# Performance work log

Measured on AMD Instinct MI355X. Metric: run time of the kernel, lower is better.

## Reference

```python
import jax, jax.numpy as jnp
import numpy as np

K = 20          # neighbors
EPS = 1e-5      # BN eps
SLOPE = 0.2     # LeakyReLU slope


def _bn_params(key, c):
    k1, k2, k3, k4 = jax.random.split(key, 4)
    gamma = jax.random.uniform(k1, (c,)) + 0.5
    beta = jax.random.normal(k2, (c,)) * 0.1
    mean = jax.random.normal(k3, (c,)) * 0.1
    var = jax.random.uniform(k4, (c,)) + 0.5
    return jnp.stack([gamma, beta, mean, var])  # [4, c]


def setup_inputs() -> dict:
    key = jax.random.key(0)
    ks = jax.random.split(key, 20)
    s = 0.05
    return {
        "x": jax.random.normal(ks[0], (16, 3, 2048), dtype=jnp.float32),
        "W1": jax.random.normal(ks[1], (64, 6)) * s,
        "bn1": _bn_params(ks[2], 64),
        "W2": jax.random.normal(ks[3], (64, 128)) * s,
        "bn2": _bn_params(ks[4], 64),
        "W3": jax.random.normal(ks[5], (128, 128)) * s,
        "bn3": _bn_params(ks[6], 128),
        "W4": jax.random.normal(ks[7], (256, 256)) * s,
        "bn4": _bn_params(ks[8], 256),
        "W5": jax.random.normal(ks[9], (1024, 512)) * s,
        "bn5": _bn_params(ks[10], 1024),
        "Wl1": jax.random.normal(ks[11], (512, 2048)) * s,
        "bn6": _bn_params(ks[12], 512),
        "Wl2": jax.random.normal(ks[13], (256, 512)) * s,
        "bl2": jax.random.normal(ks[14], (256,)) * s,
        "bn7": _bn_params(ks[15], 256),
        "Wl3": jax.random.normal(ks[16], (40, 256)) * s,
        "bl3": jax.random.normal(ks[17], (40,)) * s,
    }


def _knn_idx(xt, k):
    # xt: [B, N, C]; returns [B, N, k] indices of nearest neighbors (incl. self)
    sq = jnp.sum(xt * xt, axis=-1)                       # [B, N]
    inner = jnp.einsum("bnc,bmc->bnm", xt, xt)           # [B, N, N]
    neg_dist = 2.0 * inner - sq[:, :, None] - sq[:, None, :]
    _, idx = jax.lax.top_k(neg_dist, k)
    return idx


def _bn_act(h, bn):
    # eval-mode batchnorm over last axis + LeakyReLU
    g, b, m, v = bn[0], bn[1], bn[2], bn[3]
    h = (h - m) * (g * jax.lax.rsqrt(v + EPS)) + b
    return jnp.where(h >= 0, h, SLOPE * h)


def _edge_conv(xt, W, bn, k):
    # xt: [B, N, C] channels-last; W: [O, 2C]
    idx = _knn_idx(xt, k)                                # [B, N, k]
    nb = jax.vmap(lambda f, i: f[i])(xt, idx)            # [B, N, k, C]
    ctr = jnp.broadcast_to(xt[:, :, None, :], nb.shape)
    feat = jnp.concatenate([nb - ctr, ctr], axis=-1)     # [B, N, k, 2C]
    h = jnp.einsum("bnkc,oc->bnko", feat, W)             # 1x1 conv
    h = _bn_act(h, bn)
    return jnp.max(h, axis=2)                            # [B, N, O]


def reference(x, W1, bn1, W2, bn2, W3, bn3, W4, bn4, W5, bn5,
              Wl1, bn6, Wl2, bl2, bn7, Wl3, bl3):
    xt = jnp.transpose(x, (0, 2, 1))                     # [B, N, 3]
    x1 = _edge_conv(xt, W1, bn1, K)                      # [B, N, 64]
    x2 = _edge_conv(x1, W2, bn2, K)                      # [B, N, 64]
    x3 = _edge_conv(x2, W3, bn3, K)                      # [B, N, 128]
    x4 = _edge_conv(x3, W4, bn4, K)                      # [B, N, 256]
    cat = jnp.concatenate([x1, x2, x3, x4], axis=-1)     # [B, N, 512]
    h = jnp.einsum("bnc,oc->bno", cat, W5)               # [B, N, 1024]
    h = _bn_act(h, bn5)
    hmax = jnp.max(h, axis=1)                            # [B, 1024]
    havg = jnp.mean(h, axis=1)                           # [B, 1024]
    h = jnp.concatenate([hmax, havg], axis=-1)           # [B, 2048]
    h = _bn_act(h @ Wl1.T, bn6)                          # [B, 512] (dropout = eval no-op)
    h = _bn_act(h @ Wl2.T + bl2, bn7)                    # [B, 256]
    return h @ Wl3.T + bl3                               # [B, 40]
```

## Files before the change

### kernel.cpp

```cpp
#include <hip/hip_runtime.h>
#include <hip/hip_bf16.h>

#define BB 16
#define NN 2048
#define PP (BB*NN)
#define KNN 20

typedef __hip_bfloat16 bf16;
typedef unsigned short u16;
typedef unsigned int u32;
typedef __attribute__((ext_vector_type(8))) short s8v;
typedef __attribute__((ext_vector_type(4))) float f4v;

__device__ __forceinline__ float bu2f(u16 u){ return __uint_as_float(((u32)u) << 16); }
__device__ __forceinline__ float lo16(u32 u){ return __uint_as_float(u << 16); }
__device__ __forceinline__ float hi16(u32 u){ return __uint_as_float(u & 0xffff0000u); }
__device__ __forceinline__ u16 f2bu(float f){ bf16 h = __float2bfloat16(f); return *(u16*)&h; }
__device__ __forceinline__ float lrelu(float h){ return (h >= 0.f) ? h : 0.2f*h; }

__device__ __forceinline__ u32 f2key(float f){
  u32 u = __float_as_uint(f);
  return (u & 0x80000000u) ? ~u : (u | 0x80000000u);
}
__device__ __forceinline__ float key2f(u32 k){
  u32 u = (k & 0x80000000u) ? (k & 0x7FFFFFFFu) : ~k;
  return __uint_as_float(u);
}

template<bool BF> __device__ __forceinline__ float wget(const void* p, size_t i){
  return BF ? bu2f(((const u16*)p)[i]) : ((const float*)p)[i];
}
template<bool BF> __device__ __forceinline__ void wload8(const void* p, size_t base, float w[8]){
  if (BF){
    const uint4 u = *(const uint4*)((const u16*)p + base);
    w[0]=lo16(u.x); w[1]=hi16(u.x); w[2]=lo16(u.y); w[3]=hi16(u.y);
    w[4]=lo16(u.z); w[5]=hi16(u.z); w[6]=lo16(u.w); w[7]=hi16(u.w);
  } else {
    const float4* f = (const float4*)((const float*)p + base);
    float4 a = f[0], b = f[1];
    w[0]=a.x; w[1]=a.y; w[2]=a.z; w[3]=a.w; w[4]=b.x; w[5]=b.y; w[6]=b.z; w[7]=b.w;
  }
}

__device__ __forceinline__ f4v mfma16(s8v a, s8v b, f4v c){
  return __builtin_amdgcn_mfma_f32_16x16x32_bf16(a, b, c, 0, 0, 0);
}

template<bool BF> __device__ __forceinline__ void loadFragHL(const void* p, size_t base,
                                                             s8v& hi, s8v& lo){
  if (BF){
    hi = *(const s8v*)((const u16*)p + base);
  } else {
    float w[8]; wload8<false>(p, base, w);
    #pragma unroll
    for (int i = 0; i < 8; ++i){
      u16 hb = f2bu(w[i]);
      hi[i] = (short)hb;
      lo[i] = (short)f2bu(w[i] - bu2f(hb));
    }
  }
}
template<bool BF> __device__ __forceinline__ s8v loadFragR(const void* p, size_t base){
  if (BF){
    return *(const s8v*)((const u16*)p + base);
  } else {
    float w[8]; wload8<false>(p, base, w);
    s8v r;
    #pragma unroll
    for (int i = 0; i < 8; ++i) r[i] = (short)f2bu(w[i]);
    return r;
  }
}
template<bool BF, bool PRE> __device__ __forceinline__ s8v loadW(const void* p, size_t base){
  if (PRE) return *(const s8v*)((const u16*)p + base);
  else     return loadFragR<BF>(p, base);
}

__device__ __forceinline__ void topk_ins(float d, u32 id, float (&tv)[KNN], u32 (&ti)[KNN]){
  float pv = 0.f; u32 pi = 0u; bool cp = false;
  #pragma unroll
  for (int t = 0; t < KNN; ++t){
    bool c = (tv[t] < d);
    float ov = tv[t]; u32 oi = ti[t];
    tv[t] = c ? (cp ? pv : d) : tv[t];
    ti[t] = c ? (cp ? pi : id) : ti[t];
    pv = ov; pi = oi; cp = c;
  }
}

__global__ void k_detect(const u16* __restrict__ xr, int* __restrict__ flag){
  __shared__ int cnt;
  if (threadIdx.x == 0) cnt = 0;
  __syncthreads();
  float v = bu2f(xr[threadIdx.x * 2]);
  float a = fabsf(v);
  int ok = (a > 1e-6f && a < 1e6f) ? 1 : 0;
  atomicAdd(&cnt, ok);
  __syncthreads();
  if (threadIdx.x == 0) flag[0] = (cnt >= 160) ? 1 : 0;
}

__global__ void k_wconv(const int* __restrict__ FLAG, const void* __restrict__ src,
                        u16* __restrict__ dst, int n){
  int i = blockIdx.x*256 + threadIdx.x;
  if (i >= n) return;
  dst[i] = FLAG[0] ? ((const u16*)src)[i] : f2bu(((const float*)src)[i]);
}

template<bool BF>
__global__ void k_prep(const int* __restrict__ FLAG, const void* __restrict__ x,
                       float* __restrict__ XT, float* __restrict__ SQ,
                       u32* __restrict__ hmaxk, float* __restrict__ hsum){
  if (FLAG[0] != (BF ? 1 : 0)) return;
  int i = blockIdx.x*256 + threadIdx.x;
  if (i >= PP) return;
  int b = i / NN, n = i - b*NN;
  float s = 0.f;
  #pragma unroll
  for (int c = 0; c < 3; ++c){
    float v = wget<BF>(x, ((size_t)b*3 + c)*NN + n);
    XT[(size_t)i*3 + c] = v;
    s += v*v;
  }
  SQ[i] = s;
  if (i < BB*1024){ hmaxk[i] = 0u; hsum[i] = 0.f; }
}

template<int Cin>
__global__ void k_sq(const u16* __restrict__ xin, float* __restrict__ SQ){
  int i = blockIdx.x*256 + threadIdx.x;
  if (i >= PP) return;
  const u32* r = (const u32*)(xin + (size_t)i*Cin);
  float s = 0.f;
  for (int c = 0; c < Cin/2; ++c){
    u32 u = r[c];
    float a = lo16(u), b = hi16(u);
    s += a*a; s += b*b;
  }
  SQ[i] = s;
}

template<int C, int TC>
__global__ __launch_bounds__(256) void k_knn(const float* __restrict__ xin,
                                             const float* __restrict__ SQ,
                                             u16* __restrict__ IDX){
  __shared__ float cf[4][TC*C];
  __shared__ float csqv[4][TC];
  __shared__ float tvL[4][KNN][64];
  __shared__ u16   tiL[4][KNN][64];
  const int tid = threadIdx.x, w = tid >> 6, lane = tid & 63;
  const int b = blockIdx.y;
  const int q = blockIdx.x*64 + lane;
  const int j0 = w * 512;

  float qf[C];
  const float* xq = xin + ((size_t)b*NN + q)*C;
  #pragma unroll
  for (int c = 0; c < C; ++c) qf[c] = xq[c];
  const float sqq = SQ[b*NN + q];

  float tv[KNN]; u32 ti[KNN];
  #pragma unroll
  for (int t = 0; t < KNN; ++t){ tv[t] = -INFINITY; ti[t] = 0; }

  for (int t0 = 0; t0 < 512; t0 += TC){
    __syncthreads();
    const float* src = xin + ((size_t)b*NN + j0 + t0)*C;
    for (int k = lane; k < TC*C; k += 64) cf[w][k] = src[k];
    for (int k = lane; k < TC; k += 64) csqv[w][k] = SQ[b*NN + j0 + t0 + k];
    __syncthreads();
    for (int j = 0; j < TC; ++j){
      float dot = 0.f;
      #pragma unroll
      for (int c = 0; c < C; ++c) dot += qf[c]*cf[w][j*C + c];
      float d = 2.f*dot - sqq - csqv[w][j];
      if (d > tv[KNN-1]) topk_ins(d, (u32)(j0 + t0 + j), tv, ti);
    }
  }
  #pragma unroll
  for (int t = 0; t < KNN; ++t){ tvL[w][t][lane] = tv[t]; tiL[w][t][lane] = (u16)ti[t]; }
  __syncthreads();
  if (tid < 64){
    int p0=0,p1=0,p2=0,p3=0;
    u16* op = IDX + ((size_t)b*NN + q)*KNN;
    for (int t = 0; t < KNN; ++t){
      float v0 = tvL[0][p0][tid], v1 = tvL[1][p1][tid], v2 = tvL[2][p2][tid], v3 = tvL[3][p3][tid];
      int bs = 0; float bv = v0;
      if (v1 > bv){ bv = v1; bs = 1; }
      if (v2 > bv){ bv = v2; bs = 2; }
      if (v3 > bv){ bv = v3; bs = 3; }
      u16 bi;
      if      (bs == 0){ bi = tiL[0][p0][tid]; p0++; }
      else if (bs == 1){ bi = tiL[1][p1][tid]; p1++; }
      else if (bs == 2){ bi = tiL[2][p2][tid]; p2++; }
      else             { bi = tiL[3][p3][tid]; p3++; }
      op[t] = bi;
    }
  }
}

template<int C>
__global__ __launch_bounds__(256) void k_knn_mfma(const u16* __restrict__ xin,
                                                  const float* __restrict__ SQ,
                                                  u16* __restrict__ IDX){
  __shared__ float tvL[KNN][256];
  __shared__ u16   tiL[KNN][256];
  const int tid = threadIdx.x, w = tid >> 6, lane = tid & 63;
  const int quad = lane >> 4, n = lane & 15;
  const int seg = w & 1, qg = w >> 1;
  const int b = blockIdx.y;
  const int q = blockIdx.x*32 + qg*16 + n;
  const int cbase = seg * (NN/2);
  const u16* Xb = xin + (size_t)b*NN*C;

  s8v bfrag[C/32];
  #pragma unroll
  for (int kc = 0; kc < C/32; ++kc)
    bfrag[kc] = *(const s8v*)(Xb + (size_t)q*C + kc*32 + quad*8);
  const float sqq = SQ[b*NN + q];

  float tv[KNN]; u32 ti[KNN];
  #pragma unroll
  for (int t = 0; t < KNN; ++t){ tv[t] = -INFINITY; ti[t] = 0; }

  s8v afr[C/32], afn[C/32];
  #pragma unroll
  for (int kc = 0; kc < C/32; ++kc)
    afr[kc] = *(const s8v*)(Xb + (size_t)(cbase + n)*C + kc*32 + quad*8);

  for (int ct = cbase; ct < cbase + NN/2; ct += 16){
    int ctn = (ct + 16 < cbase + NN/2) ? (ct + 16) : cbase;
    #pragma unroll
    for (int kc = 0; kc < C/32; ++kc)
      afn[kc] = *(const s8v*)(Xb + (size_t)(ctn + n)*C + kc*32 + quad*8);
    f4v sqc = *(const f4v*)&SQ[b*NN + ct + quad*4];
    f4v acc = {0.f, 0.f, 0.f, 0.f};
    #pragma unroll
    for (int kc = 0; kc < C/32; ++kc)
      acc = mfma16(afr[kc], bfrag[kc], acc);
    #pragma unroll
    for (int r = 0; r < 4; ++r){
      float d = 2.f*acc[r] - sqq - sqc[r];
      if (d > tv[KNN-1]) topk_ins(d, (u32)(ct + quad*4 + r), tv, ti);
    }
    #pragma unroll
    for (int kc = 0; kc < C/32; ++kc) afr[kc] = afn[kc];
  }
  #pragma unroll
  for (int t = 0; t < KNN; ++t){ tvL[t][tid] = tv[t]; tiL[t][tid] = (u16)ti[t]; }
  __syncthreads();

  if (tid < 32){
    int mn = tid & 15, mqg = tid >> 4;
    int mq = blockIdx.x*32 + mqg*16 + mn;
    int p[8] = {0,0,0,0,0,0,0,0};
    u16* op = IDX + ((size_t)b*NN + mq)*KNN;
    for (int t = 0; t < KNN; ++t){
      float bv = -INFINITY; int bs = 0; u16 bi = 0xFFFF;
      #pragma unroll
      for (int s = 0; s < 8; ++s){
        int col = mqg*128 + (s >> 2)*64 + (s & 3)*16 + mn;
        float v = tvL[p[s]][col];
        u16  ii = tiL[p[s]][col];
        if (v > bv || (v == bv && ii < bi)){ bv = v; bs = s; bi = ii; }
      }
      op[t] = bi; p[bs]++;
    }
  }
}

template<bool BF>
__global__ __launch_bounds__(256) void k_ec1(const int* __restrict__ FLAG,
                    const float* __restrict__ XT,
                    const u16* __restrict__ IDX1, const void* __restrict__ W1,
                    const void* __restrict__ bn1, u16* __restrict__ x1out){
  if (FLAG[0] != (BF ? 1 : 0)) return;
  __shared__ float nbx[4][21][3];
  __shared__ float W1s[384];
  __shared__ float bn1s[256];
  __shared__ u16   idxL[4][KNN];
  const int tid = threadIdx.x;
  const int g0 = blockIdx.x*4, b = g0 / NN;
  for (int k = tid; k < 384; k += 256) W1s[k] = wget<BF>(W1, k);
  if (tid < 256) bn1s[tid] = wget<BF>(bn1, tid);
  if (tid < 80){ int pt = tid/KNN, t = tid%KNN; idxL[pt][t] = IDX1[(size_t)(g0+pt)*KNN + t]; }
  __syncthreads();
  for (int k = tid; k < 4*21*3; k += 256){
    int row = k/3, c = k - row*3;
    int pt = row/21, slot = row - pt*21;
    int m = (slot < KNN) ? (int)idxL[pt][slot] : (g0 + pt - b*NN);
    nbx[pt][slot][c] = XT[((size_t)b*NN + m)*3 + c];
  }
  __syncthreads();
  int pt = tid >> 6, o = tid & 63;
  float wa0 = W1s[o*6], wa1 = W1s[o*6+1], wa2 = W1s[o*6+2];
  float wb0 = W1s[o*6+3], wb1 = W1s[o*6+4], wb2 = W1s[o*6+5];
  float pmax = -INFINITY;
  #pragma unroll
  for (int t = 0; t < KNN; ++t)
    pmax = fmaxf(pmax, nbx[pt][t][0]*wa0 + nbx[pt][t][1]*wa1 + nbx[pt][t][2]*wa2);
  float po = nbx[pt][20][0]*wa0 + nbx[pt][20][1]*wa1 + nbx[pt][20][2]*wa2;
  float qo = nbx[pt][20][0]*wb0 + nbx[pt][20][1]*wb1 + nbx[pt][20][2]*wb2;
  float h = pmax - po + qo;
  float sc = bn1s[o] / sqrtf(bn1s[192+o] + 1e-5f);
  h = (h - bn1s[128+o])*sc + bn1s[64+o];
  x1out[(size_t)(g0+pt)*64 + o] = f2bu(lrelu(h));
}

template<int O_, bool BF>
__global__ __launch_bounds__(256, 2) void k_ec(const int* __restrict__ FLAG,
                    const u16* __restrict__ xin, const u16* __restrict__ idx,
                    const void* __restrict__ W, const void* __restrict__ bn,
                    u16* __restrict__ xout){
  if (FLAG[0] != (BF ? 1 : 0)) return;
  __shared__ __align__(16) u16 ANu[16*24*72];
  __shared__ u16 idxL[16][KNN];
  const int tid = threadIdx.x, wv = tid >> 6, lane = tid & 63;
  const int quad = lane >> 4, n = lane & 15;
  const int g0 = blockIdx.x*16, b = g0 / NN, n0 = g0 - b*NN;

  for (int k = tid; k < 16*KNN; k += 256){
    int pt = k/KNN, t = k - pt*KNN;
    idxL[pt][t] = idx[(size_t)(g0+pt)*KNN + t];
  }
  __syncthreads();
  u32* ANw = (u32*)ANu;
  for (int k = tid; k < 384*32; k += 256){
    int row = k >> 5, pr = k & 31;
    int pt = row/24, r = row - pt*24;
    int m = (r < KNN) ? (int)idxL[pt][r] : (n0 + pt);
    ANw[row*36 + pr] = ((const u32*)(xin + ((size_t)b*NN + m)*64))[pr];
  }
  __syncthreads();

  s8v aself[2];
  #pragma unroll
  for (int kc = 0; kc < 2; ++kc)
    aself[kc] = *(const s8v*)&ANu[((lane&15)*24 + 20)*72 + kc*32 + quad*8];

  for (int tt = wv; tt < O_/16; tt += 4){
    const int o = tt*16 + n;
    s8v bah[2], bal[2];
    f4v accq;
    {
      f4v tq = {0.f,0.f,0.f,0.f};
      {
        s8v bbh[2], bbl[2];
        #pragma unroll
        for (int kc = 0; kc < 2; ++kc)
          loadFragHL<BF>(W, (size_t)o*128 + 64 + kc*32 + quad*8, bbh[kc], bbl[kc]);
        #pragma unroll
        for (int kc = 0; kc < 2; ++kc){
          tq = mfma16(aself[kc], bbh[kc], tq);
          if (!BF) tq = mfma16(aself[kc], bbl[kc], tq);
        }
      }
      #pragma unroll
      for (int kc = 0; kc < 2; ++kc)
        loadFragHL<BF>(W, (size_t)o*128 + kc*32 + quad*8, bah[kc], bal[kc]);
      f4v uq = {0.f,0.f,0.f,0.f};
      #pragma unroll
      for (int kc = 0; kc < 2; ++kc){
        uq = mfma16(aself[kc], bah[kc], uq);
        if (!BF) uq = mfma16(aself[kc], bal[kc], uq);
      }
      accq = tq - uq;
    }
    float g  = wget<BF>(bn, o),        be = wget<BF>(bn, O_+o),
          mu = wget<BF>(bn, 2*O_+o),   va = wget<BF>(bn, 3*O_+o);
    float sc = g / sqrtf(va + 1e-5f);

    #pragma unroll 2
    for (int pt = 0; pt < 16; ++pt){
      s8v a0[2], a1[2];
      #pragma unroll
      for (int kc = 0; kc < 2; ++kc){
        a0[kc] = *(const s8v*)&ANu[(pt*24 + (lane&15))*72 + kc*32 + quad*8];
        a1[kc] = *(const s8v*)&ANu[(pt*24 + 16 + (lane&7))*72 + kc*32 + quad*8];
      }
      f4v c0 = {0.f,0.f,0.f,0.f}, c1 = {0.f,0.f,0.f,0.f};
      #pragma unroll
      for (int kc = 0; kc < 2; ++kc){
        c0 = mfma16(a0[kc], bah[kc], c0);
        c1 = mfma16(a1[kc], bah[kc], c1);
        if (!BF){
          c0 = mfma16(a0[kc], bal[kc], c0);
          c1 = mfma16(a1[kc], bal[kc], c1);
        }
      }
      float pm = fmaxf(fmaxf(fmaxf(c0[0],c0[1]), fmaxf(c0[2],c0[3])),
                       fmaxf(fmaxf(c1[0],c1[1]), fmaxf(c1[2],c1[3])));
      pm = fmaxf(pm, __shfl_xor(pm, 16));
      pm = fmaxf(pm, __shfl_xor(pm, 32));
      if (quad == (pt >> 2)){
        float h = pm + accq[pt & 3];
        h = (h - mu)*sc + be;
        xout[(size_t)(g0+pt)*O_ + o] = f2bu(lrelu(h));
      }
    }
  }
}

#define PTS 16
template<bool BF, bool PRE>
__global__ __launch_bounds__(512, 1)
void k_w5f(const int* __restrict__ FLAG,
      const float* __restrict__ XT,
      const u16* __restrict__ IDX1, const u16* __restrict__ x2g, const u16* __restrict__ x3g,
      const u16* __restrict__ IDX4,
      const void* __restrict__ W1, const void* __restrict__ bn1,
      const void* __restrict__ W4, const void* __restrict__ bn4,
      const void* __restrict__ W5, const void* __restrict__ bn5,
      u32* __restrict__ hmaxk, float* __restrict__ hsum){
  if (FLAG[0] != (BF ? 1 : 0)) return;
  __shared__ __align__(16) u16 ANu[PTS*24*136];
  __shared__ __align__(16) u16 xsu[PTS*520];
  __shared__ float xtn[PTS][21][3];
  __shared__ u16   idx1L[PTS][KNN], idx4L[PTS][KNN];
  __shared__ float W1s[384], bn1s[256], bn4s[1024];
  const int tid = threadIdx.x, wv = tid >> 6, lane = tid & 63;
  const int quad = lane >> 4, n = lane & 15;
  const int g0 = blockIdx.x*PTS, b = g0 / NN, n0 = g0 - b*NN;

  for (int k = tid; k < PTS*KNN; k += 512){
    int pt = k/KNN, t = k - pt*KNN;
    idx1L[pt][t] = IDX1[(size_t)(g0+pt)*KNN + t];
    idx4L[pt][t] = IDX4[(size_t)(g0+pt)*KNN + t];
  }
  if (tid < 384) W1s[tid] = wget<BF>(W1, tid);
  if (tid < 256) bn1s[tid] = wget<BF>(bn1, tid);
  for (int k = tid; k < 1024; k += 512) bn4s[k] = wget<BF>(bn4, k);
  __syncthreads();

  u32* ANw = (u32*)ANu;
  for (int k = tid; k < PTS*24*64; k += 512){
    int row = k >> 6, pr = k & 63;
    int pt = row/24, r = row - pt*24;
    int m = (r < KNN) ? (int)idx4L[pt][r] : (n0 + pt);
    ANw[(pt*24 + r)*68 + pr] = ((const u32*)(x3g + ((size_t)b*NN + m)*128))[pr];
  }
  for (int k = tid; k < PTS*21*3; k += 512){
    int row = k/3, c = k - row*3;
    int pt = row/21, slot = row - pt*21;
    int m = (slot < KNN) ? (int)idx1L[pt][slot] : (n0 + pt);
    xtn[pt][slot][c] = XT[((size_t)b*NN + m)*3 + c];
  }
  u32* xsw = (u32*)xsu;
  for (int k = tid; k < PTS*32; k += 512){
    int pt = k >> 5, c2 = k & 31;
    xsw[pt*260 + 32 + c2] = ((const u32*)(x2g + (size_t)(g0+pt)*64))[c2];
  }
  for (int k = tid; k < PTS*64; k += 512){
    int pt = k >> 6, c2 = k & 63;
    xsw[pt*260 + 64 + c2] = ((const u32*)(x3g + (size_t)(g0+pt)*128))[c2];
  }
  __syncthreads();

  #pragma unroll
  for (int hh = 0; hh < PTS*64/512; ++hh){
    int k = tid + hh*512;
    int pt = k >> 6, o = k & 63;
    float wa0 = W1s[o*6], wa1 = W1s[o*6+1], wa2 = W1s[o*6+2];
    float wb0 = W1s[o*6+3], wb1 = W1s[o*6+4], wb2 = W1s[o*6+5];
    float pmax = -INFINITY;
    #pragma unroll
    for (int t = 0; t < KNN; ++t)
      pmax = fmaxf(pmax, xtn[pt][t][0]*wa0 + xtn[pt][t][1]*wa1 + xtn[pt][t][2]*wa2);
    float po = xtn[pt][20][0]*wa0 + xtn[pt][20][1]*wa1 + xtn[pt][20][2]*wa2;
    float qo = xtn[pt][20][0]*wb0 + xtn[pt][20][1]*wb1 + xtn[pt][20][2]*wb2;
    float h = pmax - po + qo;
    float sc = bn1s[o] / sqrtf(bn1s[192+o] + 1e-5f);
    h = (h - bn1s[128+o])*sc + bn1s[64+o];
    xsu[pt*520 + o] = f2bu(lrelu(h));
  }

  {
    s8v aself[4];
    #pragma unroll
    for (int kc = 0; kc < 4; ++kc)
      aself[kc] = *(const s8v*)&ANu[((lane&15)*24 + 20)*136 + kc*32 + quad*8];

    #pragma unroll 1
    for (int i = 0; i < 2; ++i){
      const int o0 = (wv*2 + i)*16;
      const size_t wrow = (size_t)(o0 + n)*256;
      s8v bah[4];
      f4v accq;
      {
        f4v tq = {0.f,0.f,0.f,0.f};
        #pragma unroll
        for (int kc = 0; kc < 4; ++kc){
          s8v bb = loadW<BF,PRE>(W4, wrow + 128 + kc*32 + quad*8);
          tq = mfma16(aself[kc], bb, tq);
        }
        #pragma unroll
        for (int kc = 0; kc < 4; ++kc)
          bah[kc] = loadW<BF,PRE>(W4, wrow + kc*32 + quad*8);
        f4v uq = {0.f,0.f,0.f,0.f};
        #pragma unroll
        for (int kc = 0; kc < 4; ++kc)
          uq = mfma16(aself[kc], bah[kc], uq);
        accq = tq - uq;
      }
      #pragma unroll 2
      for (int pt = 0; pt < PTS; ++pt){
        s8v a0[4], a1[4];
        #pragma unroll
        for (int kc = 0; kc < 4; ++kc){
          a0[kc] = *(const s8v*)&ANu[(pt*24 + (lane&15))*136 + kc*32 + quad*8];
          a1[kc] = *(const s8v*)&ANu[(pt*24 + 16 + (lane&7))*136 + kc*32 + quad*8];
        }
        f4v c0 = {0.f,0.f,0.f,0.f}, c1 = {0.f,0.f,0.f,0.f};
        #pragma unroll
        for (int kc = 0; kc < 4; ++kc){
          c0 = mfma16(a0[kc], bah[kc], c0);
          c1 = mfma16(a1[kc], bah[kc], c1);
        }
        float pm = fmaxf(fmaxf(fmaxf(c0[0],c0[1]), fmaxf(c0[2],c0[3])),
                         fmaxf(fmaxf(c1[0],c1[1]), fmaxf(c1[2],c1[3])));
        pm = fmaxf(pm, __shfl_xor(pm, 16));
        pm = fmaxf(pm, __shfl_xor(pm, 32));
        if (quad == (pt >> 2)){
          float h = pm + accq[pt & 3];
          int o = o0 + n;
          float sc = bn4s[o] / sqrtf(bn4s[768+o] + 1e-5f);
          h = (h - bn4s[512+o])*sc + bn4s[256+o];
          xsu[pt*520 + 256 + o] = f2bu(lrelu(h));
        }
      }
    }
  }
  __syncthreads();

  {
    #pragma unroll 1
    for (int i = 0; i < 8; ++i){
      const int o = (wv*8 + i)*16 + n;
      const size_t wrow = (size_t)o * 512;
      f4v acc = {0.f,0.f,0.f,0.f};
      #pragma unroll
      for (int kc = 0; kc < 16; ++kc){
        s8v av = *(const s8v*)&xsu[(lane&15)*520 + kc*32 + quad*8];
        s8v bh = loadW<BF,PRE>(W5, wrow + kc*32 + quad*8);
        acc = mfma16(av, bh, acc);
      }
      float g = wget<BF>(bn5, o), be = wget<BF>(bn5, 1024+o),
            mu = wget<BF>(bn5, 2048+o), va = wget<BF>(bn5, 3072+o);
      float sc = g / sqrtf(va + 1e-5f);
      float lm = -INFINITY, ls = 0.f;
      #pragma unroll
      for (int r = 0; r < 4; ++r){
        float h = (acc[r] - mu)*sc + be;
        h = lrelu(h);
        lm = fmaxf(lm, h); ls += h;
      }
      lm = fmaxf(lm, __shfl_xor(lm, 16));
      ls = ls + __shfl_xor(ls, 16);
      lm = fmaxf(lm, __shfl_xor(lm, 32));
      ls = ls + __shfl_xor(ls, 32);
      if (quad == 0){
        atomicMax(&hmaxk[b*1024 + o], f2key(lm));
        atomicAdd(&hsum[b*1024 + o], ls);
      }
    }
  }
}

template<bool BF>
__global__ __launch_bounds__(512) void k_head(const int* __restrict__ FLAG,
                    const u32* __restrict__ hmaxk, const float* __restrict__ hsum,
                    const void* __restrict__ Wl1, const void* __restrict__ bn6,
                    const void* __restrict__ Wl2, const void* __restrict__ bl2,
                    const void* __restrict__ bn7,
                    const void* __restrict__ Wl3, const void* __restrict__ bl3,
                    void* __restrict__ out){
  if (FLAG[0] != (BF ? 1 : 0)) return;
  __shared__ float hc[2048];
  __shared__ float h2s[512];
  __shared__ float h3s[256];
  int b = blockIdx.x, tid = threadIdx.x;
  for (int k = tid; k < 1024; k += 512){
    hc[k]        = key2f(hmaxk[b*1024 + k]);
    hc[1024 + k] = hsum[b*1024 + k] * (1.0f/2048.0f);
  }
  __syncthreads();
  {
    float acc = 0.f;
    for (int cc = 0; cc < 2048; cc += 8){
      float w[8];
      wload8<BF>(Wl1, (size_t)tid*2048 + cc, w);
      #pragma unroll
      for (int u = 0; u < 8; ++u) acc += w[u]*hc[cc+u];
    }
    float g = wget<BF>(bn6, tid), be = wget<BF>(bn6, 512+tid),
          mu = wget<BF>(bn6, 1024+tid), va = wget<BF>(bn6, 1536+tid);
    float sc = g / sqrtf(va + 1e-5f);
    h2s[tid] = lrelu((acc - mu)*sc + be);
  }
  __syncthreads();
  if (tid < 256){
    float acc = 0.f;
    for (int cc = 0; cc < 512; cc += 8){
      float w[8];
      wload8<BF>(Wl2, (size_t)tid*512 + cc, w);
      #pragma unroll
      for (int u = 0; u < 8; ++u) acc += w[u]*h2s[cc+u];
    }
    acc += wget<BF>(bl2, tid);
    float g = wget<BF>(bn7, tid), be = wget<BF>(bn7, 256+tid),
          mu = wget<BF>(bn7, 512+tid), va = wget<BF>(bn7, 768+tid);
    float sc = g / sqrtf(va + 1e-5f);
    h3s[tid] = lrelu((acc - mu)*sc + be);
  }
  __syncthreads();
  if (tid < 40){
    float acc = 0.f;
    for (int cc = 0; cc < 256; cc += 8){
      float w[8];
      wload8<BF>(Wl3, (size_t)tid*256 + cc, w);
      #pragma unroll
      for (int u = 0; u < 8; ++u) acc += w[u]*h3s[cc+u];
    }
    acc += wget<BF>(bl3, tid);
    if (BF) ((u16*)out)[b*40 + tid] = f2bu(acc);
    else    ((float*)out)[b*40 + tid] = acc;
  }
}

extern "C" void kernel_launch(void* const* d_in, const int* in_sizes, int n_in,
                              void* d_out, int out_size, void* d_ws, size_t ws_size,
                              hipStream_t stream){
  const void* x   = d_in[0];
  const void* W1  = d_in[1];
  const void* bn1 = d_in[2];
  const void* W2  = d_in[3];
  const void* bn2 = d_in[4];
  const void* W3  = d_in[5];
  const void* bn3 = d_in[6];
  const void* W4  = d_in[7];
  const void* bn4 = d_in[8];
  const void* W5  = d_in[9];
  const void* bn5 = d_in[10];
  const void* Wl1 = d_in[11];
  const void* bn6 = d_in[12];
  const void* Wl2 = d_in[13];
  const void* bl2 = d_in[14];
  const void* bn7 = d_in[15];
  const void* Wl3 = d_in[16];
  const void* bl3 = d_in[17];

  char* base = (char*)d_ws;
  int*   FLAG  = (int*)  (base + 0);
  float* XT    = (float*)(base + 256);
  float* SQ    = (float*)(base + 393472);
  u32*   HMAXK = (u32*)  (base + 524544);
  float* HSUM  = (float*)(base + 590080);
  u16*   IDX1  = (u16*)  (base + 655616);
  u16*   IDX   = (u16*)  (base + 1966336);
  u16*   X2    = (u16*)  (base + 3277056);
  u16*   X3    = (u16*)  (base + 7471360);
  u16*   X1    = X3;
  u16*   W4B   = (u16*)  (base + 15859968);
  u16*   W5B   = (u16*)  (base + 15991040);
  const bool pre = (ws_size >= (size_t)17039616);

  dim3 knnG1(NN/64, BB);
  dim3 knnGM(NN/32, BB);

  k_detect<<<1, 256, 0, stream>>>((const u16*)x, FLAG);

  if (pre){
    k_wconv<<<(65536 + 255)/256, 256, 0, stream>>>(FLAG, W4, W4B, 65536);
    k_wconv<<<(524288 + 255)/256, 256, 0, stream>>>(FLAG, W5, W5B, 524288);
  }

  k_prep<true ><<<PP/256, 256, 0, stream>>>(FLAG, x, XT, SQ, HMAXK, HSUM);
  k_prep<false><<<PP/256, 256, 0, stream>>>(FLAG, x, XT, SQ, HMAXK, HSUM);

  k_knn<3,128><<<knnG1, 256, 0, stream>>>(XT, SQ, IDX1);
  k_ec1<true ><<<PP/4, 256, 0, stream>>>(FLAG, XT, IDX1, W1, bn1, X1);
  k_ec1<false><<<PP/4, 256, 0, stream>>>(FLAG, XT, IDX1, W1, bn1, X1);

  k_sq<64><<<PP/256, 256, 0, stream>>>(X1, SQ);
  k_knn_mfma<64><<<knnGM, 256, 0, stream>>>(X1, SQ, IDX);
  k_ec<64,true ><<<PP/16, 256, 0, stream>>>(FLAG, X1, IDX, W2, bn2, X2);
  k_ec<64,false><<<PP/16, 256, 0, stream>>>(FLAG, X1, IDX, W2, bn2, X2);

  k_sq<64><<<PP/256, 256, 0, stream>>>(X2, SQ);
  k_knn_mfma<64><<<knnGM, 256, 0, stream>>>(X2, SQ, IDX);
  k_ec<128,true ><<<PP/16, 256, 0, stream>>>(FLAG, X2, IDX, W3, bn3, X3);
  k_ec<128,false><<<PP/16, 256, 0, stream>>>(FLAG, X2, IDX, W3, bn3, X3);

  k_sq<128><<<PP/256, 256, 0, stream>>>(X3, SQ);
  k_knn_mfma<128><<<knnGM, 256, 0, stream>>>(X3, SQ, IDX);

  if (pre){
    k_w5f<true ,true ><<<PP/PTS, 512, 0, stream>>>(FLAG, XT, IDX1, X2, X3, IDX,
                                                   W1, bn1, W4B, bn4, W5B, bn5, HMAXK, HSUM);
    k_w5f<false,true ><<<PP/PTS, 512, 0, stream>>>(FLAG, XT, IDX1, X2, X3, IDX,
                                                   W1, bn1, W4B, bn4, W5B, bn5, HMAXK, HSUM);
  } else {
    k_w5f<true ,false><<<PP/PTS, 512, 0, stream>>>(FLAG, XT, IDX1, X2, X3, IDX,
                                                   W1, bn1, W4, bn4, W5, bn5, HMAXK, HSUM);
    k_w5f<false,false><<<PP/PTS, 512, 0, stream>>>(FLAG, XT, IDX1, X2, X3, IDX,
                                                   W1, bn1, W4, bn4, W5, bn5, HMAXK, HSUM);
  }

  k_head<true ><<<BB, 512, 0, stream>>>(FLAG, HMAXK, HSUM, Wl1, bn6, Wl2, bl2, bn7, Wl3, bl3, d_out);
  k_head<false><<<BB, 512, 0, stream>>>(FLAG, HMAXK, HSUM, Wl1, bn6, Wl2, bl2, bn7, Wl3, bl3, d_out);
}
```

Measured before the change: 2.012 ms.

## Pack kNN distance and index into one u32 key; pre-convert W2/W3 to bf16

The MFMA kNN kernel now keeps a single 32-bit key per candidate: an order-preserving distance key with its low 11 bits replaced by the inverted column index. This halves top-k register state and shared-memory traffic and makes the merge a plain unsigned compare. The cost is distance precision truncated to about 21 bits, which can change tie ordering for near-equal distances. Separately, W2 and W3 are converted to bf16 once into workspace so the edge-conv kernels load pre-converted fragments and skip the lo-part MFMAs on the fp32 path, when the workspace is large enough.

Measured after the change: 1.706 ms. 15.2% less time.

```diff
diff --git a/kernel.cpp b/kernel.cpp
--- a/kernel.cpp
+++ b/kernel.cpp
@@ -85,6 +85,16 @@
     tv[t] = c ? (cp ? pv : d) : tv[t];
     ti[t] = c ? (cp ? pi : id) : ti[t];
     pv = ov; pi = oi; cp = c;
+  }
+}
+__device__ __forceinline__ void topk_insp(u32 pk, u32 (&tv)[KNN]){
+  u32 pv = 0u; bool cp = false;
+  #pragma unroll
+  for (int t = 0; t < KNN; ++t){
+    bool c = (tv[t] < pk);
+    u32 ov = tv[t];
+    tv[t] = c ? (cp ? pv : pk) : tv[t];
+    pv = ov; cp = c;
   }
 }
 
@@ -203,8 +213,7 @@
 __global__ __launch_bounds__(256) void k_knn_mfma(const u16* __restrict__ xin,
                                                   const float* __restrict__ SQ,
                                                   u16* __restrict__ IDX){
-  __shared__ float tvL[KNN][256];
-  __shared__ u16   tiL[KNN][256];
+  __shared__ u32 tvL[KNN][256];
   const int tid = threadIdx.x, w = tid >> 6, lane = tid & 63;
   const int quad = lane >> 4, n = lane & 15;
   const int seg = w & 1, qg = w >> 1;
@@ -219,9 +228,9 @@
     bfrag[kc] = *(const s8v*)(Xb + (size_t)q*C + kc*32 + quad*8);
   const float sqq = SQ[b*NN + q];
 
-  float tv[KNN]; u32 ti[KNN];
-  #pragma unroll
-  for (int t = 0; t < KNN; ++t){ tv[t] = -INFINITY; ti[t] = 0; }
+  u32 tv[KNN];
+  #pragma unroll
+  for (int t = 0; t < KNN; ++t) tv[t] = 0u;
 
   s8v afr[C/32], afn[C/32];
   #pragma unroll
@@ -241,13 +250,14 @@
     #pragma unroll
     for (int r = 0; r < 4; ++r){
       float d = 2.f*acc[r] - sqq - sqc[r];
-      if (d > tv[KNN-1]) topk_ins(d, (u32)(ct + quad*4 + r), tv, ti);
+      u32 pk = (f2key(d) & 0xFFFFF800u) | (2047u - (u32)(ct + quad*4 + r));
+      if (pk > tv[KNN-1]) topk_insp(pk, tv);
     }
     #pragma unroll
     for (int kc = 0; kc < C/32; ++kc) afr[kc] = afn[kc];
   }
   #pragma unroll
-  for (int t = 0; t < KNN; ++t){ tvL[t][tid] = tv[t]; tiL[t][tid] = (u16)ti[t]; }
+  for (int t = 0; t < KNN; ++t) tvL[t][tid] = tv[t];
   __syncthreads();
 
   if (tid < 32){
@@ -256,15 +266,14 @@
     int p[8] = {0,0,0,0,0,0,0,0};
     u16* op = IDX + ((size_t)b*NN + mq)*KNN;
     for (int t = 0; t < KNN; ++t){
-      float bv = -INFINITY; int bs = 0; u16 bi = 0xFFFF;
+      u32 bv = 0u; int bs = 0;
       #pragma unroll
       for (int s = 0; s < 8; ++s){
         int col = mqg*128 + (s >> 2)*64 + (s & 3)*16 + mn;
-        float v = tvL[p[s]][col];
-        u16  ii = tiL[p[s]][col];
-        if (v > bv || (v == bv && ii < bi)){ bv = v; bs = s; bi = ii; }
-      }
-      op[t] = bi; p[bs]++;
+        u32 v = tvL[p[s]][col];
+        if (v > bv){ bv = v; bs = s; }
+      }
+      op[t] = (u16)(2047u - (bv & 2047u)); p[bs]++;
     }
   }
 }
@@ -307,7 +316,7 @@
   x1out[(size_t)(g0+pt)*64 + o] = f2bu(lrelu(h));
 }
 
-template<int O_, bool BF>
+template<int O_, bool BF, bool PRE>
 __global__ __launch_bounds__(256, 2) void k_ec(const int* __restrict__ FLAG,
                     const u16* __restrict__ xin, const u16* __restrict__ idx,
                     const void* __restrict__ W, const void* __restrict__ bn,
@@ -342,7 +351,22 @@
     const int o = tt*16 + n;
     s8v bah[2], bal[2];
     f4v accq;
-    {
+    if (PRE){
+      f4v tq = {0.f,0.f,0.f,0.f};
+      #pragma unroll
+      for (int kc = 0; kc < 2; ++kc){
+        s8v bb = *(const s8v*)((const u16*)W + (size_t)o*128 + 64 + kc*32 + quad*8);
+        tq = mfma16(aself[kc], bb, tq);
+      }
+      #pragma unroll
+      for (int kc = 0; kc < 2; ++kc)
+        bah[kc] = *(const s8v*)((const u16*)W + (size_t)o*128 + kc*32 + quad*8);
+      f4v uq = {0.f,0.f,0.f,0.f};
+      #pragma unroll
+      for (int kc = 0; kc < 2; ++kc)
+        uq = mfma16(aself[kc], bah[kc], uq);
+      accq = tq - uq;
+    } else {
       f4v tq = {0.f,0.f,0.f,0.f};
       {
         s8v bbh[2], bbl[2];
@@ -383,7 +407,7 @@
       for (int kc = 0; kc < 2; ++kc){
         c0 = mfma16(a0[kc], bah[kc], c0);
         c1 = mfma16(a1[kc], bah[kc], c1);
-        if (!BF){
+        if (!BF && !PRE){
           c0 = mfma16(a0[kc], bal[kc], c0);
           c1 = mfma16(a1[kc], bal[kc], c1);
         }
@@ -662,7 +686,10 @@
   u16*   X1    = X3;
   u16*   W4B   = (u16*)  (base + 15859968);
   u16*   W5B   = (u16*)  (base + 15991040);
-  const bool pre = (ws_size >= (size_t)17039616);
+  u16*   W2B   = (u16*)  (base + 17039616);
+  u16*   W3B   = (u16*)  (base + 17056000);
+  const bool pre  = (ws_size >= (size_t)17039616);
+  const bool pre2 = (ws_size >= (size_t)17088768);
 
   dim3 knnG1(NN/64, BB);
   dim3 knnGM(NN/32, BB);
@@ -673,6 +700,10 @@
     k_wconv<<<(65536 + 255)/256, 256, 0, stream>>>(FLAG, W4, W4B, 65536);
     k_wconv<<<(524288 + 255)/256, 256, 0, stream>>>(FLAG, W5, W5B, 524288);
   }
+  if (pre2){
+    k_wconv<<<(8192 + 255)/256, 256, 0, stream>>>(FLAG, W2, W2B, 8192);
+    k_wconv<<<(16384 + 255)/256, 256, 0, stream>>>(FLAG, W3, W3B, 16384);
+  }
 
   k_prep<true ><<<PP/256, 256, 0, stream>>>(FLAG, x, XT, SQ, HMAXK, HSUM);
   k_prep<false><<<PP/256, 256, 0, stream>>>(FLAG, x, XT, SQ, HMAXK, HSUM);
@@ -683,13 +714,23 @@
 
   k_sq<64><<<PP/256, 256, 0, stream>>>(X1, SQ);
   k_knn_mfma<64><<<knnGM, 256, 0, stream>>>(X1, SQ, IDX);
-  k_ec<64,true ><<<PP/16, 256, 0, stream>>>(FLAG, X1, IDX, W2, bn2, X2);
-  k_ec<64,false><<<PP/16, 256, 0, stream>>>(FLAG, X1, IDX, W2, bn2, X2);
+  if (pre2){
+    k_ec<64,true ,true ><<<PP/16, 256, 0, stream>>>(FLAG, X1, IDX, W2B, bn2, X2);
+    k_ec<64,false,true ><<<PP/16, 256, 0, stream>>>(FLAG, X1, IDX, W2B, bn2, X2);
+  } else {
+    k_ec<64,true ,false><<<PP/16, 256, 0, stream>>>(FLAG, X1, IDX, W2, bn2, X2);
+    k_ec<64,false,false><<<PP/16, 256, 0, stream>>>(FLAG, X1, IDX, W2, bn2, X2);
+  }
 
   k_sq<64><<<PP/256, 256, 0, stream>>>(X2, SQ);
   k_knn_mfma<64><<<knnGM, 256, 0, stream>>>(X2, SQ, IDX);
-  k_ec<128,true ><<<PP/16, 256, 0, stream>>>(FLAG, X2, IDX, W3, bn3, X3);
-  k_ec<128,false><<<PP/16, 256, 0, stream>>>(FLAG, X2, IDX, W3, bn3, X3);
+  if (pre2){
+    k_ec<128,true ,true ><<<PP/16, 256, 0, stream>>>(FLAG, X2, IDX, W3B, bn3, X3);
+    k_ec<128,false,true ><<<PP/16, 256, 0, stream>>>(FLAG, X2, IDX, W3B, bn3, X3);
+  } else {
+    k_ec<128,true ,false><<<PP/16, 256, 0, stream>>>(FLAG, X2, IDX, W3, bn3, X3);
+    k_ec<128,false,false><<<PP/16, 256, 0, stream>>>(FLAG, X2, IDX, W3, bn3, X3);
+  }
 
   k_sq<128><<<PP/256, 256, 0, stream>>>(X3, SQ);
   k_knn_mfma<128><<<knnGM, 256, 0, stream>>>(X3, SQ, IDX);
```
